# Performance work log

Measured on AMD Instinct MI355X. Metric: run time of the kernel, lower is better.

Reference implementation:

```python
import jax, jax.numpy as jnp
import numpy as np

B, L, DIM = 4, 2048, 1024
EXPAND, D_STATE, D_CONV = 2, 16, 4
D_INNER = EXPAND * DIM          # 2048
DT_RANK = DIM // 16             # 64
MLP_HID = 4 * DIM


def setup_inputs() -> dict:
    key = jax.random.key(0)
    ks = jax.random.split(key, 20)
    s = 0.02
    inp = {
        "hidden_states": jax.random.normal(ks[0], (B, L, DIM), jnp.float32),
        "cond": jax.random.normal(ks[1], (B, DIM), jnp.float32),
        # norm (LayerNorm with affine)
        "norm_w": jnp.ones((DIM,), jnp.float32),
        "norm_b": jnp.zeros((DIM,), jnp.float32),
        # adaLN: Linear(dim, 6*dim)
        "ada_w": jax.random.normal(ks[2], (6 * DIM, DIM), jnp.float32) * s,
        "ada_b": jnp.zeros((6 * DIM,), jnp.float32),
        # Mamba mixer params
        "in_proj_w": jax.random.normal(ks[3], (2 * D_INNER, DIM), jnp.float32) * s,
        "conv_w": jax.random.normal(ks[4], (D_INNER, 1, D_CONV), jnp.float32) * s,
        "conv_b": jnp.zeros((D_INNER,), jnp.float32),
        "x_proj_w": jax.random.normal(ks[5], (DT_RANK + 2 * D_STATE, D_INNER), jnp.float32) * s,
        "dt_proj_w": jax.random.normal(ks[6], (D_INNER, DT_RANK), jnp.float32) * s,
        "dt_proj_b": jax.random.uniform(ks[7], (D_INNER,), jnp.float32, -4.0, -2.0),
        "A_log": jnp.log(jnp.broadcast_to(jnp.arange(1, D_STATE + 1, dtype=jnp.float32), (D_INNER, D_STATE))),
        "Dp": jnp.ones((D_INNER,), jnp.float32),
        "out_proj_w": jax.random.normal(ks[8], (DIM, D_INNER), jnp.float32) * s,
        # MLP
        "fc1_w": jax.random.normal(ks[9], (MLP_HID, DIM), jnp.float32) * s,
        "fc1_b": jnp.zeros((MLP_HID,), jnp.float32),
        "fc2_w": jax.random.normal(ks[10], (DIM, MLP_HID), jnp.float32) * s,
        "fc2_b": jnp.zeros((DIM,), jnp.float32),
    }
    return inp


def _layernorm(x, w, b, eps):
    mu = jnp.mean(x, axis=-1, keepdims=True)
    var = jnp.mean(jnp.square(x - mu), axis=-1, keepdims=True)
    y = (x - mu) * jax.lax.rsqrt(var + eps)
    return y * w + b if w is not None else y


def _modulate(x, shift, scale):
    # x: [B,L,D]; shift/scale: [B,D]
    return x * (1.0 + scale[:, None, :]) + shift[:, None, :]


def _mamba(x_in, in_proj_w, conv_w, conv_b, x_proj_w, dt_proj_w, dt_proj_b, A_log, Dp, out_proj_w):
    # x_in: [B,L,DIM]
    xz = jnp.einsum("bld,ed->ble", x_in, in_proj_w)        # [B,L,2*Di]
    x, z = jnp.split(xz, 2, axis=-1)                        # each [B,L,Di]
    # causal depthwise conv over L
    x_ncl = jnp.transpose(x, (0, 2, 1))                     # [B,Di,L]
    x_ncl = jax.lax.conv_general_dilated(
        x_ncl, conv_w, window_strides=(1,), padding=[(D_CONV - 1, 0)],
        feature_group_count=D_INNER, dimension_numbers=("NCH", "OIH", "NCH"))
    x = jnp.transpose(x_ncl, (0, 2, 1)) + conv_b            # [B,L,Di]
    x = jax.nn.silu(x)
    x_dbl = jnp.einsum("bld,ed->ble", x, x_proj_w)          # [B,L,dt_rank+2*N]
    dt, Bm, Cm = jnp.split(x_dbl, [DT_RANK, DT_RANK + D_STATE], axis=-1)
    dt = jax.nn.softplus(jnp.einsum("blr,dr->bld", dt, dt_proj_w) + dt_proj_b)  # [B,L,Di]
    A = -jnp.exp(A_log)                                     # [Di,N]

    def step(h, inps):
        dt_t, B_t, C_t, x_t = inps                          # [B,Di],[B,N],[B,N],[B,Di]
        dA = jnp.exp(dt_t[..., None] * A)                   # [B,Di,N]
        dBx = (dt_t * x_t)[..., None] * B_t[:, None, :]     # [B,Di,N]
        h = h * dA + dBx
        y = jnp.einsum("bdn,bn->bd", h, C_t)
        return h, y

    h0 = jnp.zeros((x.shape[0], D_INNER, D_STATE), x.dtype)
    xs = (jnp.transpose(dt, (1, 0, 2)), jnp.transpose(Bm, (1, 0, 2)),
          jnp.transpose(Cm, (1, 0, 2)), jnp.transpose(x, (1, 0, 2)))
    _, ys = jax.lax.scan(step, h0, xs)                      # [L,B,Di]
    y = jnp.transpose(ys, (1, 0, 2)) + x * Dp               # [B,L,Di]
    y = y * jax.nn.silu(z)
    return jnp.einsum("bld,od->blo", y, out_proj_w)         # [B,L,DIM]


def reference(hidden_states, cond, norm_w, norm_b, ada_w, ada_b, in_proj_w, conv_w,
              conv_b, x_proj_w, dt_proj_w, dt_proj_b, A_log, Dp, out_proj_w,
              fc1_w, fc1_b, fc2_w, fc2_b):
    residual = hidden_states                                # residual=None path
    hs = _layernorm(residual, norm_w, norm_b, 1e-5)
    mods = jax.nn.silu(cond) @ ada_w.T + ada_b              # [B,6*DIM]
    shift_msa, scale_msa, gate_msa, shift_mlp, scale_mlp, gate_mlp = jnp.split(mods, 6, axis=1)
    hs = gate_msa[:, None, :] * _mamba(_modulate(hs, shift_msa, scale_msa),
                                       in_proj_w, conv_w, conv_b, x_proj_w,
                                       dt_proj_w, dt_proj_b, A_log, Dp, out_proj_w)
    h2 = _modulate(_layernorm(hs, None, None, 1e-6), shift_mlp, scale_mlp)
    h2 = jax.nn.gelu(h2 @ fc1_w.T + fc1_b, approximate=True) @ fc2_w.T + fc2_b
    hs = hs + gate_mlp[:, None, :] * h2
    return (hs, residual)
```

## Files before the change

kernel.cpp:

```cpp
#include <hip/hip_runtime.h>
#include <hip/hip_bf16.h>


typedef unsigned short ushort_t;
typedef __attribute__((ext_vector_type(8))) short short8;
typedef __attribute__((ext_vector_type(4))) float floatx4;
typedef __attribute__((ext_vector_type(4))) unsigned short ushort4v;

#define DEVI __device__ __forceinline__

DEVI float b2f(ushort_t u) { union { unsigned int i; float f; } v; v.i = ((unsigned int)u) << 16; return v.f; }
DEVI ushort_t f2b(float f) {
    union { float f; unsigned int i; } v; v.f = f;
    unsigned int r = v.i + 0x7fffu + ((v.i >> 16) & 1u);
    return (ushort_t)(r >> 16);
}
DEVI float sigmoidf_(float x) { return 1.f / (1.f + __expf(-x)); }
DEVI float siluf_(float x) { return x * sigmoidf_(x); }
DEVI float softplusf_(float x) { return (x > 20.f) ? x : log1pf(__expf(x)); }
DEVI float gelu_tanh_(float x) {
    float c = 0.7978845608028654f * (x + 0.044715f * x * x * x);
    return 0.5f * x * (1.f + tanhf(c));
}
DEVI void async16(ushort_t* lds, const ushort_t* g) {
    __builtin_amdgcn_global_load_lds((const __attribute__((address_space(1))) void*)g,
                                     (__attribute__((address_space(3))) void*)lds,
                                     16, 0, 0);
}

__global__ void detect_kernel(const void* norm_w, int* flag) {
    if (threadIdx.x == 0)
        flag[0] = (((const unsigned int*)norm_w)[0] == 0x3F800000u) ? 1 : 0;
}

__global__ __launch_bounds__(256) void convert_w_kernel(
    const void* __restrict__ src, ushort_t* __restrict__ dst, int n8,
    const int* __restrict__ flag)
{
    int i = blockIdx.x * 256 + threadIdx.x;
    if (i >= n8) return;
    if (*flag) {
        const float4* s = (const float4*)src;
        float4 a = s[2 * i], b = s[2 * i + 1];
        short8 o;
        o[0] = (short)f2b(a.x); o[1] = (short)f2b(a.y);
        o[2] = (short)f2b(a.z); o[3] = (short)f2b(a.w);
        o[4] = (short)f2b(b.x); o[5] = (short)f2b(b.y);
        o[6] = (short)f2b(b.z); o[7] = (short)f2b(b.w);
        ((short8*)dst)[i] = o;
    } else {
        ((short8*)dst)[i] = ((const short8*)src)[i];
    }
}

__global__ __launch_bounds__(256) void canon_bias_kernel(
    const void* __restrict__ src, float* __restrict__ dst, int n,
    const int* __restrict__ flag)
{
    int i = blockIdx.x * 256 + threadIdx.x;
    if (i >= n) return;
    dst[i] = (*flag) ? ((const float*)src)[i] : b2f(((const ushort_t*)src)[i]);
}

__global__ __launch_bounds__(256) void residual_kernel(
    const void* __restrict__ src, void* __restrict__ dst, const int* __restrict__ flag)
{
    size_t i = (size_t)blockIdx.x * 256 + threadIdx.x;
    if (*flag) {
        ((float4*)((float*)dst + 8388608))[i] = ((const float4*)src)[i];
    } else {
        ((ushort4v*)((ushort_t*)dst + 8388608))[i] = ((const ushort4v*)src)[i];
    }
}

__global__ __launch_bounds__(256) void ada_kernel(
    const void* __restrict__ condv, const void* __restrict__ ada_wv,
    const void* __restrict__ ada_bv, float* __restrict__ mods,
    const int* __restrict__ flag)
{
    __shared__ float sc[4096];
    const int tid = threadIdx.x;
    const bool f32 = (*flag != 0);
    if (f32) {
        const float* cf = (const float*)condv;
        for (int i = tid; i < 4096; i += 256) sc[i] = siluf_(cf[i]);
    } else {
        const ushort_t* cb = (const ushort_t*)condv;
        for (int i = tid; i < 4096; i += 256) sc[i] = siluf_(b2f(cb[i]));
    }
    __syncthreads();
    const int j = blockIdx.x * 256 + tid;
    float bb = f32 ? ((const float*)ada_bv)[j] : b2f(((const ushort_t*)ada_bv)[j]);
    float s0 = bb, s1 = bb, s2 = bb, s3 = bb;
    if (f32) {
        const float4* w4 = ((const float4*)ada_wv) + (size_t)j * 256;
        for (int d4 = 0; d4 < 256; d4++) {
            float4 w = w4[d4];
            float wv[4] = {w.x, w.y, w.z, w.w};
#pragma unroll
            for (int e = 0; e < 4; e++) {
                int d = d4 * 4 + e;
                s0 += sc[d] * wv[e];
                s1 += sc[1024 + d] * wv[e];
                s2 += sc[2048 + d] * wv[e];
                s3 += sc[3072 + d] * wv[e];
            }
        }
    } else {
        const ushort_t* wrow = ((const ushort_t*)ada_wv) + (size_t)j * 1024;
        for (int d = 0; d < 1024; d += 8) {
            short8 w8 = *(const short8*)(wrow + d);
#pragma unroll
            for (int e = 0; e < 8; e++) {
                float wv = b2f(((const ushort_t*)&w8)[e]);
                s0 += sc[d + e] * wv;
                s1 += sc[1024 + d + e] * wv;
                s2 += sc[2048 + d + e] * wv;
                s3 += sc[3072 + d + e] * wv;
            }
        }
    }
    mods[0 * 6144 + j] = s0;
    mods[1 * 6144 + j] = s1;
    mods[2 * 6144 + j] = s2;
    mods[3 * 6144 + j] = s3;
}

__global__ __launch_bounds__(256) void ln1_mod_kernel(
    const void* __restrict__ hiddenv, const void* __restrict__ nwv,
    const void* __restrict__ nbv, const float* __restrict__ mods,
    ushort_t* __restrict__ xout, const int* __restrict__ flag)
{
    const int t = blockIdx.x, tid = threadIdx.x;
    const int bb = t >> 11;
    const bool f32 = (*flag != 0);
    float vv[4], s = 0.f, ss = 0.f;
    if (f32) {
        float4 u = ((const float4*)((const float*)hiddenv + (size_t)t * 1024))[tid];
        vv[0] = u.x; vv[1] = u.y; vv[2] = u.z; vv[3] = u.w;
    } else {
        ushort4v u = ((const ushort4v*)((const ushort_t*)hiddenv + (size_t)t * 1024))[tid];
#pragma unroll
        for (int j = 0; j < 4; j++) vv[j] = b2f(u[j]);
    }
#pragma unroll
    for (int j = 0; j < 4; j++) { s += vv[j]; ss += vv[j] * vv[j]; }
#pragma unroll
    for (int off = 32; off > 0; off >>= 1) { s += __shfl_down(s, off); ss += __shfl_down(ss, off); }
    __shared__ float red[8];
    const int wave = tid >> 6, lane = tid & 63;
    if (lane == 0) { red[wave] = s; red[4 + wave] = ss; }
    __syncthreads();
    s = red[0] + red[1] + red[2] + red[3];
    ss = red[4] + red[5] + red[6] + red[7];
    const float mu = s * (1.f / 1024.f);
    const float var = ss * (1.f / 1024.f) - mu * mu;
    const float rstd = rsqrtf(var + 1e-5f);
    const float* mrow = mods + (size_t)bb * 6144;
    ushort4v o;
#pragma unroll
    for (int j = 0; j < 4; j++) {
        int d = tid * 4 + j;
        float w = f32 ? ((const float*)nwv)[d] : b2f(((const ushort_t*)nwv)[d]);
        float b = f32 ? ((const float*)nbv)[d] : b2f(((const ushort_t*)nbv)[d]);
        float y = (vv[j] - mu) * rstd * w + b;
        y = y * (1.f + mrow[1024 + d]) + mrow[d];
        o[j] = f2b(y);
    }
    ((ushort4v*)(xout + (size_t)t * 1024))[tid] = o;
}

__global__ __launch_bounds__(256) void ln2_mod_kernel(
    const ushort_t* __restrict__ hs, const float* __restrict__ mods,
    ushort_t* __restrict__ xout)
{
    const int t = blockIdx.x, tid = threadIdx.x;
    const int bb = t >> 11;
    ushort4v u = ((const ushort4v*)(hs + (size_t)t * 1024))[tid];
    float vv[4], s = 0.f, ss = 0.f;
#pragma unroll
    for (int j = 0; j < 4; j++) { vv[j] = b2f(u[j]); s += vv[j]; ss += vv[j] * vv[j]; }
#pragma unroll
    for (int off = 32; off > 0; off >>= 1) { s += __shfl_down(s, off); ss += __shfl_down(ss, off); }
    __shared__ float red[8];
    const int wave = tid >> 6, lane = tid & 63;
    if (lane == 0) { red[wave] = s; red[4 + wave] = ss; }
    __syncthreads();
    s = red[0] + red[1] + red[2] + red[3];
    ss = red[4] + red[5] + red[6] + red[7];
    const float mu = s * (1.f / 1024.f);
    const float var = ss * (1.f / 1024.f) - mu * mu;
    const float rstd = rsqrtf(var + 1e-6f);
    const float* mrow = mods + (size_t)bb * 6144;
    ushort4v o;
#pragma unroll
    for (int j = 0; j < 4; j++) {
        int d = tid * 4 + j;
        float y = (vv[j] - mu) * rstd;
        y = y * (1.f + mrow[4096 + d]) + mrow[3072 + d];
        o[j] = f2b(y);
    }
    ((ushort4v*)(xout + (size_t)t * 1024))[tid] = o;
}

__global__ __launch_bounds__(256) void conv_silu_kernel(
    const ushort_t* __restrict__ xb, const void* __restrict__ cwv,
    const void* __restrict__ cbv, ushort_t* __restrict__ xc,
    const int* __restrict__ flag)
{
    const int t = blockIdx.x;
    const int l = t & 2047;
    const int c0 = threadIdx.x * 8;
    const bool f32 = (*flag != 0);
    float acc[8];
    float wlf[32];
    if (f32) {
        const float* cbf = (const float*)cbv;
#pragma unroll
        for (int j = 0; j < 8; j++) acc[j] = cbf[c0 + j];
        const float4* cw4 = (const float4*)((const float*)cwv + (size_t)c0 * 4);
#pragma unroll
        for (int q = 0; q < 8; q++) {
            float4 w = cw4[q];
            wlf[q * 4 + 0] = w.x; wlf[q * 4 + 1] = w.y;
            wlf[q * 4 + 2] = w.z; wlf[q * 4 + 3] = w.w;
        }
    } else {
        const ushort_t* cbb = (const ushort_t*)cbv;
#pragma unroll
        for (int j = 0; j < 8; j++) acc[j] = b2f(cbb[c0 + j]);
        const ushort_t* cwb = (const ushort_t*)cwv + (size_t)c0 * 4;
#pragma unroll
        for (int q = 0; q < 32; q++) wlf[q] = b2f(cwb[q]);
    }
#pragma unroll
    for (int k = 0; k < 4; k++) {
        int tl = l + k - 3;
        if (tl < 0) continue;
        short8 xv = *(const short8*)(xb + (size_t)(t + k - 3) * 2048 + c0);
#pragma unroll
        for (int j = 0; j < 8; j++)
            acc[j] += b2f(((const ushort_t*)&xv)[j]) * wlf[j * 4 + k];
    }
    short8 o;
#pragma unroll
    for (int j = 0; j < 8; j++) ((ushort_t*)&o)[j] = f2b(siluf_(acc[j]));
    *(short8*)(xc + (size_t)t * 2048 + c0) = o;
}

__global__ __launch_bounds__(256) void scan_phase1(
    const ushort_t* __restrict__ dtb, const ushort_t* __restrict__ xcv,
    const ushort_t* __restrict__ xdbl, const void* __restrict__ A_logv,
    ushort_t* __restrict__ Hloc, ushort_t* __restrict__ Pst,
    const int* __restrict__ flag)
{
    const int blk = blockIdx.x;
    const int dblk = blk & 7;
    const int c = (blk >> 3) & 31;
    const int b = blk >> 8;
    const int d = dblk * 256 + threadIdx.x;
    const bool f32 = (*flag != 0);
    float Av[16];
#pragma unroll
    for (int n = 0; n < 16; n++) {
        float al = f32 ? ((const float*)A_logv)[(size_t)d * 16 + n]
                       : b2f(((const ushort_t*)A_logv)[(size_t)d * 16 + n]);
        Av[n] = -__expf(al);
    }
    float h[16], Pa[16];
#pragma unroll
    for (int n = 0; n < 16; n++) { h[n] = 0.f; Pa[n] = 1.f; }
    const int t0 = c * 64;
    size_t tb = ((size_t)b * 2048 + t0) * 2048 + d;
    float dtv = b2f(dtb[tb]);
    float xv  = b2f(xcv[tb]);
    for (int tt = 0; tt < 64; ++tt) {
        float dtn = b2f(dtb[tb + 2048]);
        float xn  = b2f(xcv[tb + 2048]);
        const ushort_t* bp = xdbl + ((size_t)b * 2048 + t0 + tt) * 96 + 64;
        short8 B8a = *(const short8*)bp;
        short8 B8b = *(const short8*)(bp + 8);
        float dtx = dtv * xv;
#pragma unroll
        for (int n = 0; n < 8; n++) {
            float dA = __expf(dtv * Av[n]);
            h[n] = h[n] * dA + dtx * b2f(((const ushort_t*)&B8a)[n]);
            Pa[n] *= dA;
        }
#pragma unroll
        for (int n = 8; n < 16; n++) {
            float dA = __expf(dtv * Av[n]);
            h[n] = h[n] * dA + dtx * b2f(((const ushort_t*)&B8b)[n - 8]);
            Pa[n] *= dA;
        }
        dtv = dtn; xv = xn; tb += 2048;
    }
    const size_t o = (((size_t)c * 4 + b) * 16) * 2048 + d;
#pragma unroll
    for (int n = 0; n < 16; n++) {
        Hloc[o + (size_t)n * 2048] = f2b(h[n]);
        Pst [o + (size_t)n * 2048] = f2b(Pa[n]);
    }
}

__global__ __launch_bounds__(256) void scan_phase2(
    const ushort_t* __restrict__ Hloc, const ushort_t* __restrict__ Pst,
    float* __restrict__ Hin)
{
    const int gi = blockIdx.x * 256 + threadIdx.x;
    const int d = gi & 2047;
    const int n = (gi >> 11) & 15;
    const int b = gi >> 15;
    float h = 0.f;
    const size_t o0 = ((size_t)b * 16 + n) * 2048 + d;
    for (int c = 0; c < 32; ++c) {
        const size_t o = o0 + (size_t)c * (4 * 16 * 2048);
        Hin[o] = h;
        h = b2f(Hloc[o]) + b2f(Pst[o]) * h;
    }
}

__global__ __launch_bounds__(256) void scan_phase3(
    const ushort_t* __restrict__ dtb, ushort_t* __restrict__ xc,
    const ushort_t* __restrict__ xdbl, const ushort_t* __restrict__ zbuf,
    const void* __restrict__ A_logv, const void* __restrict__ Dpv,
    const float* __restrict__ Hin, const int* __restrict__ flag)
{
    const int blk = blockIdx.x;
    const int dblk = blk & 7;
    const int c = (blk >> 3) & 31;
    const int b = blk >> 8;
    const int d = dblk * 256 + threadIdx.x;
    const bool f32 = (*flag != 0);
    float Av[16];
#pragma unroll
    for (int n = 0; n < 16; n++) {
        float al = f32 ? ((const float*)A_logv)[(size_t)d * 16 + n]
                       : b2f(((const ushort_t*)A_logv)[(size_t)d * 16 + n]);
        Av[n] = -__expf(al);
    }
    const float Dv = f32 ? ((const float*)Dpv)[d] : b2f(((const ushort_t*)Dpv)[d]);
    float h[16];
    {
        const size_t o = (((size_t)c * 4 + b) * 16) * 2048 + d;
#pragma unroll
        for (int n = 0; n < 16; n++) h[n] = Hin[o + (size_t)n * 2048];
    }
    const int t0 = c * 64;
    size_t tb = ((size_t)b * 2048 + t0) * 2048 + d;
    float dtv = b2f(dtb[tb]);
    float xv  = b2f(xc[tb]);
    float zv  = b2f(zbuf[tb]);
    for (int tt = 0; tt < 64; ++tt) {
        float dtn = b2f(dtb[tb + 2048]);
        float xn  = b2f(xc[tb + 2048]);
        float zn  = b2f(zbuf[tb + 2048]);
        const ushort_t* bp = xdbl + ((size_t)b * 2048 + t0 + tt) * 96 + 64;
        short8 B8a = *(const short8*)bp;
        short8 B8b = *(const short8*)(bp + 8);
        short8 C8a = *(const short8*)(bp + 16);
        short8 C8b = *(const short8*)(bp + 24);
        float dtx = dtv * xv;
        float y = 0.f;
#pragma unroll
        for (int n = 0; n < 8; n++) {
            float dA = __expf(dtv * Av[n]);
            h[n] = h[n] * dA + dtx * b2f(((const ushort_t*)&B8a)[n]);
            y += h[n] * b2f(((const ushort_t*)&C8a)[n]);
        }
#pragma unroll
        for (int n = 8; n < 16; n++) {
            float dA = __expf(dtv * Av[n]);
            h[n] = h[n] * dA + dtx * b2f(((const ushort_t*)&B8b)[n - 8]);
            y += h[n] * b2f(((const ushort_t*)&C8b)[n - 8]);
        }
        float yo = (y + xv * Dv) * siluf_(zv);
        xc[tb] = f2b(yo);
        dtv = dtn; xv = xn; zv = zn; tb += 2048;
    }
}

template <int EPI>
DEVI void epi_store(int row, int col, float v,
                    void* C0, void* C1, int ldc,
                    const float* bias, const float* mods,
                    const ushort_t* hs, int fl)
{
    if constexpr (EPI == 0) {
        if (col < 2048)
            ((ushort_t*)C0)[(size_t)row * 2048 + col] = f2b(v);
        else
            ((ushort_t*)C1)[(size_t)row * 2048 + (col - 2048)] = f2b(v);
    } else if constexpr (EPI == 1) {
        ((ushort_t*)C0)[(size_t)row * ldc + col] = f2b(v);
    } else if constexpr (EPI == 2) {
        v += bias[col];
        ((ushort_t*)C0)[(size_t)row * ldc + col] = f2b(softplusf_(v));
    } else if constexpr (EPI == 3) {
        const int bb = row >> 11;
        v *= mods[(size_t)bb * 6144 + 2048 + col];
        ((ushort_t*)C0)[(size_t)row * ldc + col] = f2b(v);
    } else if constexpr (EPI == 4) {
        v += bias[col];
        ((ushort_t*)C0)[(size_t)row * ldc + col] = f2b(gelu_tanh_(v));
    } else if constexpr (EPI == 5) {
        v += bias[col];
        const int bb = row >> 11;
        float o = b2f(hs[(size_t)row * 1024 + col]) + mods[(size_t)bb * 6144 + 5120 + col] * v;
        if (fl)
            ((float*)C0)[(size_t)row * ldc + col] = o;
        else
            ((ushort_t*)C0)[(size_t)row * ldc + col] = f2b(o);
    }
}

template <int EPI>
__global__ __launch_bounds__(256) void gemm_bt(
    const ushort_t* __restrict__ A, int lda,
    const ushort_t* __restrict__ W,
    int M, int N, int K,
    void* __restrict__ C0, void* __restrict__ C1, int ldc,
    const float* __restrict__ bias,
    const float* __restrict__ mods,
    const ushort_t* __restrict__ hs,
    const int* __restrict__ flag)
{
    __shared__ __align__(16) ushort_t sA[2][128 * 64];
    __shared__ __align__(16) ushort_t sB[2][128 * 64];
    const int tid = threadIdx.x;
    const int wave = tid >> 6, lane = tid & 63;
    const int Mt = M >> 7;
    int bid = blockIdx.x;
    { const int cpx = (int)gridDim.x >> 3; bid = (bid & 7) * cpx + (bid >> 3); }
    const int mt = bid % Mt, nt = bid / Mt;
    const int m0 = mt << 7, n0 = nt << 7;
    const int wr = wave >> 1, wc = wave & 1;
    const int r = tid >> 3, c8 = tid & 7;
    const int rs7 = r & 7;
    int fl = 0;
    if constexpr (EPI == 5) fl = *flag;

    floatx4 acc[4][4];
#pragma unroll
    for (int m = 0; m < 4; m++)
#pragma unroll
        for (int nn = 0; nn < 4; nn++) acc[m][nn] = floatx4{0.f, 0.f, 0.f, 0.f};

    auto stage = [&](int buf, int kt) {
        const int kb = kt << 6;
#pragma unroll
        for (int i = 0; i < 4; i++) {
            const int row = i * 32 + r;
            async16(&sA[buf][(size_t)row * 64 + c8 * 8],
                    A + (size_t)(m0 + row) * lda + kb + ((c8 ^ rs7) << 3));
            int rB = n0 + row; if (rB >= N) rB = N - 1;
            async16(&sB[buf][(size_t)row * 64 + c8 * 8],
                    W + (size_t)rB * K + kb + ((c8 ^ rs7) << 3));
        }
    };
    auto compute = [&](int buf) {
#pragma unroll
        for (int kk = 0; kk < 2; kk++) {
            const int sw = ((kk * 4 + (lane >> 4)) ^ (lane & 7)) << 3;
            short8 bfr[4];
#pragma unroll
            for (int nn = 0; nn < 4; nn++)
                bfr[nn] = *(const short8*)&sB[buf][(size_t)(wc * 64 + nn * 16 + (lane & 15)) * 64 + sw];
#pragma unroll
            for (int m = 0; m < 4; m++) {
                short8 af = *(const short8*)&sA[buf][(size_t)(wr * 64 + m * 16 + (lane & 15)) * 64 + sw];
#pragma unroll
                for (int nn = 0; nn < 4; nn++)
                    acc[m][nn] = __builtin_amdgcn_mfma_f32_16x16x32_bf16(af, bfr[nn], acc[m][nn], 0, 0, 0);
            }
        }
    };

    const int NT = K >> 6;
    stage(0, 0);
    __syncthreads();
    int cur = 0;
    for (int kt = 0; kt < NT - 1; kt++) {
        stage(cur ^ 1, kt + 1);
        compute(cur);
        __syncthreads();
        cur ^= 1;
    }
    compute(cur);

    const int erow = wr * 64 + ((lane >> 4) << 2);
    const int ecol = wc * 64 + (lane & 15);
#pragma unroll
    for (int m = 0; m < 4; m++)
#pragma unroll
        for (int nn = 0; nn < 4; nn++) {
            const int col = n0 + ecol + nn * 16;
            if (col >= N) continue;
#pragma unroll
            for (int rr = 0; rr < 4; rr++)
                epi_store<EPI>(m0 + erow + m * 16 + rr, col, acc[m][nn][rr],
                               C0, C1, ldc, bias, mods, hs, fl);
        }
}

template <int EPI>
__global__ __launch_bounds__(512) void gemm256(
    const ushort_t* __restrict__ A, int lda,
    const ushort_t* __restrict__ W,
    int M, int N, int K,
    void* __restrict__ C0, void* __restrict__ C1, int ldc,
    const float* __restrict__ bias,
    const float* __restrict__ mods,
    const ushort_t* __restrict__ hs,
    const int* __restrict__ flag)
{
    __shared__ __align__(16) ushort_t sA[2][256 * 64];
    __shared__ __align__(16) ushort_t sB[2][256 * 64];
    const int tid = threadIdx.x;
    const int wave = tid >> 6, lane = tid & 63;
    const int Mt = M >> 8;
    int bid = blockIdx.x;
    { const int cpx = (int)gridDim.x >> 3; bid = (bid & 7) * cpx + (bid >> 3); }
    const int mt = bid % Mt, nt = bid / Mt;
    const int m0 = mt << 8, n0 = nt << 8;
    const int wr = wave >> 2, wc = wave & 3;
    const int r = tid >> 3, c8 = tid & 7;
    const int rs7 = r & 7;
    int fl = 0;
    if constexpr (EPI == 5) fl = *flag;

    floatx4 acc[8][4];
#pragma unroll
    for (int m = 0; m < 8; m++)
#pragma unroll
        for (int nn = 0; nn < 4; nn++) acc[m][nn] = floatx4{0.f, 0.f, 0.f, 0.f};

    auto stage = [&](int buf, int kt) {
        const int kb = kt << 6;
#pragma unroll
        for (int i = 0; i < 4; i++) {
            const int row = i * 64 + r;
            async16(&sA[buf][(size_t)row * 64 + c8 * 8],
                    A + (size_t)(m0 + row) * lda + kb + ((c8 ^ rs7) << 3));
            async16(&sB[buf][(size_t)row * 64 + c8 * 8],
                    W + (size_t)(n0 + row) * K + kb + ((c8 ^ rs7) << 3));
        }
    };
    auto compute = [&](int buf) {
#pragma unroll
        for (int kk = 0; kk < 2; kk++) {
            const int sw = ((kk * 4 + (lane >> 4)) ^ (lane & 7)) << 3;
            short8 bfr[4];
#pragma unroll
            for (int nn = 0; nn < 4; nn++)
                bfr[nn] = *(const short8*)&sB[buf][(size_t)(wc * 64 + nn * 16 + (lane & 15)) * 64 + sw];
#pragma unroll
            for (int m = 0; m < 8; m++) {
                short8 af = *(const short8*)&sA[buf][(size_t)(wr * 128 + m * 16 + (lane & 15)) * 64 + sw];
#pragma unroll
                for (int nn = 0; nn < 4; nn++)
                    acc[m][nn] = __builtin_amdgcn_mfma_f32_16x16x32_bf16(af, bfr[nn], acc[m][nn], 0, 0, 0);
            }
        }
    };

    const int NT = K >> 6;
    stage(0, 0);
    __syncthreads();
    int cur = 0;
    for (int kt = 0; kt < NT - 1; kt++) {
        stage(cur ^ 1, kt + 1);
        compute(cur);
        __syncthreads();
        cur ^= 1;
    }
    compute(cur);

    const int erow = wr * 128 + ((lane >> 4) << 2);
    const int ecol = wc * 64 + (lane & 15);
#pragma unroll
    for (int m = 0; m < 8; m++)
#pragma unroll
        for (int nn = 0; nn < 4; nn++) {
            const int col = n0 + ecol + nn * 16;
            if (col >= N) continue;
#pragma unroll
            for (int rr = 0; rr < 4; rr++)
                epi_store<EPI>(m0 + erow + m * 16 + rr, col, acc[m][nn][rr],
                               C0, C1, ldc, bias, mods, hs, fl);
        }
}

extern "C" void kernel_launch(void* const* d_in, const int* in_sizes, int n_in,
                              void* d_out, int out_size, void* d_ws, size_t ws_size,
                              hipStream_t stream)
{
    const void* hidden   = d_in[0];
    const void* cond     = d_in[1];
    const void* norm_w   = d_in[2];
    const void* norm_b   = d_in[3];
    const void* ada_w    = d_in[4];
    const void* ada_b    = d_in[5];
    const void* in_proj  = d_in[6];
    const void* conv_w   = d_in[7];
    const void* conv_b   = d_in[8];
    const void* x_proj   = d_in[9];
    const void* dt_w     = d_in[10];
    const void* dt_b     = d_in[11];
    const void* A_log    = d_in[12];
    const void* Dp       = d_in[13];
    const void* out_proj = d_in[14];
    const void* fc1_w    = d_in[15];
    const void* fc1_b    = d_in[16];
    const void* fc2_w    = d_in[17];
    const void* fc2_b    = d_in[18];

    constexpr size_t OFF_FLAG  = 0;
    constexpr size_t OFF_MODS  = 256;
    constexpr size_t OFF_DTB_F = 131072;
    constexpr size_t OFF_FC1B  = 139264;
    constexpr size_t OFF_FC2B  = 155648;
    constexpr size_t OFF_WIN   = 262144;
    constexpr size_t OFF_WXP   = 8650752;
    constexpr size_t OFF_WDT   = 9043968;
    constexpr size_t OFF_WOUT  = 9306112;
    constexpr size_t OFF_WFC1  = 13500416;
    constexpr size_t OFF_WFC2  = 21889024;
    constexpr size_t OFF_XBUF  = 30277632;
    constexpr size_t OFF_ZBUF  = 63832064;
    constexpr size_t OFF_XCONV = 97386496;
    constexpr size_t OFF_XIN   = 130940928;
    constexpr size_t OFF_XDBL  = 147718144;
    constexpr size_t OFF_HS    = 149291008;
    constexpr size_t WS_NEED   = 166068224;
    if (ws_size < WS_NEED) return;

    char* ws = (char*)d_ws;
    int*      flag   = (int*)(ws + OFF_FLAG);
    float*    mods   = (float*)(ws + OFF_MODS);
    float*    dtb_f  = (float*)(ws + OFF_DTB_F);
    float*    fc1b_f = (float*)(ws + OFF_FC1B);
    float*    fc2b_f = (float*)(ws + OFF_FC2B);
    ushort_t* w_in   = (ushort_t*)(ws + OFF_WIN);
    ushort_t* w_xp   = (ushort_t*)(ws + OFF_WXP);
    ushort_t* w_dt   = (ushort_t*)(ws + OFF_WDT);
    ushort_t* w_out  = (ushort_t*)(ws + OFF_WOUT);
    ushort_t* w_fc1  = (ushort_t*)(ws + OFF_WFC1);
    ushort_t* w_fc2  = (ushort_t*)(ws + OFF_WFC2);
    ushort_t* xbuf   = (ushort_t*)(ws + OFF_XBUF);
    ushort_t* zbuf   = (ushort_t*)(ws + OFF_ZBUF);
    ushort_t* x_conv = (ushort_t*)(ws + OFF_XCONV);
    ushort_t* x_in   = (ushort_t*)(ws + OFF_XIN);
    ushort_t* x_dbl  = (ushort_t*)(ws + OFF_XDBL);
    ushort_t* hsb    = (ushort_t*)(ws + OFF_HS);
    ushort_t* dtb    = xbuf;
    ushort_t* h1     = xbuf;
    ushort_t* h2in   = x_in;
    ushort_t* Hloc   = (ushort_t*)(ws + OFF_XIN);
    ushort_t* Pst    = (ushort_t*)(ws + OFF_XIN + 8388608);
    float*    Hin    = (float*)(ws + OFF_HS);

    detect_kernel<<<1, 64, 0, stream>>>(norm_w, flag);

    convert_w_kernel<<<2048, 256, 0, stream>>>(in_proj, w_in, 524288, flag);
    convert_w_kernel<<<96, 256, 0, stream>>>(x_proj, w_xp, 24576, flag);
    convert_w_kernel<<<64, 256, 0, stream>>>(dt_w, w_dt, 16384, flag);
    convert_w_kernel<<<1024, 256, 0, stream>>>(out_proj, w_out, 262144, flag);
    convert_w_kernel<<<2048, 256, 0, stream>>>(fc1_w, w_fc1, 524288, flag);
    convert_w_kernel<<<2048, 256, 0, stream>>>(fc2_w, w_fc2, 524288, flag);
    canon_bias_kernel<<<8, 256, 0, stream>>>(dt_b, dtb_f, 2048, flag);
    canon_bias_kernel<<<16, 256, 0, stream>>>(fc1_b, fc1b_f, 4096, flag);
    canon_bias_kernel<<<4, 256, 0, stream>>>(fc2_b, fc2b_f, 1024, flag);

    residual_kernel<<<8192, 256, 0, stream>>>(hidden, d_out, flag);

    ada_kernel<<<24, 256, 0, stream>>>(cond, ada_w, ada_b, mods, flag);
    ln1_mod_kernel<<<8192, 256, 0, stream>>>(hidden, norm_w, norm_b, mods, x_in, flag);
    gemm256<0><<<32 * 16, 512, 0, stream>>>(x_in, 1024, w_in, 8192, 4096, 1024,
                                            xbuf, zbuf, 2048, nullptr, nullptr, nullptr, flag);
    conv_silu_kernel<<<8192, 256, 0, stream>>>(xbuf, conv_w, conv_b, x_conv, flag);
    gemm_bt<1><<<64 * 1, 256, 0, stream>>>(x_conv, 2048, w_xp, 8192, 96, 2048,
                                           x_dbl, nullptr, 96, nullptr, nullptr, nullptr, flag);
    gemm_bt<2><<<64 * 16, 256, 0, stream>>>(x_dbl, 96, w_dt, 8192, 2048, 64,
                                            dtb, nullptr, 2048, dtb_f, nullptr, nullptr, flag);
    scan_phase1<<<1024, 256, 0, stream>>>(dtb, x_conv, x_dbl, A_log, Hloc, Pst, flag);
    scan_phase2<<<512, 256, 0, stream>>>(Hloc, Pst, Hin);
    scan_phase3<<<1024, 256, 0, stream>>>(dtb, x_conv, x_dbl, zbuf, A_log, Dp, Hin, flag);
    gemm_bt<3><<<64 * 8, 256, 0, stream>>>(x_conv, 2048, w_out, 8192, 1024, 2048,
                                           hsb, nullptr, 1024, nullptr, mods, nullptr, flag);
    ln2_mod_kernel<<<8192, 256, 0, stream>>>(hsb, mods, h2in);
    gemm256<4><<<32 * 16, 512, 0, stream>>>(h2in, 1024, w_fc1, 8192, 4096, 1024,
                                            h1, nullptr, 4096, fc1b_f, nullptr, nullptr, flag);
    gemm_bt<5><<<64 * 8, 256, 0, stream>>>(h1, 4096, w_fc2, 8192, 1024, 4096,
                                           d_out, nullptr, 1024, fc2b_f, mods, hsb, flag);
}
```

Before: 787.4 us.

## Pipeline GEMM K-loop with explicit vmcnt waits and 8x8 tile swizzle

Replaces the double-buffered GEMM K-loop's __syncthreads with explicit s_waitcnt vmcnt(8) plus raw s_barrier and priority raising around the MFMA compute. Global-to-LDS prefetch of the next tile can then stay in flight while the current tile is consumed. Also remaps workgroup IDs into 8x8 tile groups within each XCD-strided slice to improve L2 reuse of A and W panels. The vmcnt count assumes each thread issues exactly 8 loads per stage, which is fragile if the stage load count differs between the two GEMM variants.

```diff
diff --git a/kernel.cpp b/kernel.cpp
--- a/kernel.cpp
+++ b/kernel.cpp
@@ -26,6 +26,21 @@
     __builtin_amdgcn_global_load_lds((const __attribute__((address_space(1))) void*)g,
                                      (__attribute__((address_space(3))) void*)lds,
                                      16, 0, 0);
+}
+
+DEVI void remap_tile(int bid, int Mt, int Nt, int& mt, int& nt) {
+    const int nwg = Mt * Nt;
+    const int cpx = nwg >> 3;
+    const int v = (bid & 7) * cpx + (bid >> 3);
+    if (((Mt & 7) == 0) && ((Nt & 7) == 0)) {
+        const int s = v >> 6, w = v & 63;
+        const int smt = s % (Mt >> 3), snt = s / (Mt >> 3);
+        mt = smt * 8 + (w >> 3);
+        nt = snt * 8 + (w & 7);
+    } else {
+        mt = v % Mt;
+        nt = v / Mt;
+    }
 }
 
 __global__ void detect_kernel(const void* norm_w, int* flag) {
@@ -414,6 +429,30 @@
     }
 }
 
+#define KLOOP_PIPE(NT)                                               \
+    stage(0, 0);                                                     \
+    {                                                                \
+        int cur = 0;                                                 \
+        for (int kt = 0; kt < (NT); kt++) {                          \
+            if (kt + 1 < (NT)) {                                     \
+                stage(cur ^ 1, kt + 1);                              \
+                asm volatile("s_waitcnt vmcnt(8)" ::: "memory");     \
+            } else {                                                 \
+                asm volatile("s_waitcnt vmcnt(0)" ::: "memory");     \
+            }                                                        \
+            __builtin_amdgcn_sched_barrier(0);                       \
+            __builtin_amdgcn_s_barrier();                            \
+            __builtin_amdgcn_sched_barrier(0);                       \
+            __builtin_amdgcn_s_setprio(1);                           \
+            compute(cur);                                            \
+            __builtin_amdgcn_s_setprio(0);                           \
+            __builtin_amdgcn_sched_barrier(0);                       \
+            __builtin_amdgcn_s_barrier();                            \
+            __builtin_amdgcn_sched_barrier(0);                       \
+            cur ^= 1;                                                \
+        }                                                            \
+    }
+
 template <int EPI>
 __global__ __launch_bounds__(256) void gemm_bt(
     const ushort_t* __restrict__ A, int lda,
@@ -429,10 +468,8 @@
     __shared__ __align__(16) ushort_t sB[2][128 * 64];
     const int tid = threadIdx.x;
     const int wave = tid >> 6, lane = tid & 63;
-    const int Mt = M >> 7;
-    int bid = blockIdx.x;
-    { const int cpx = (int)gridDim.x >> 3; bid = (bid & 7) * cpx + (bid >> 3); }
-    const int mt = bid % Mt, nt = bid / Mt;
+    int mt, nt;
+    remap_tile(blockIdx.x, M >> 7, (N + 127) >> 7, mt, nt);
     const int m0 = mt << 7, n0 = nt << 7;
     const int wr = wave >> 1, wc = wave & 1;
     const int r = tid >> 3, c8 = tid & 7;
@@ -477,16 +514,7 @@
     };
 
     const int NT = K >> 6;
-    stage(0, 0);
-    __syncthreads();
-    int cur = 0;
-    for (int kt = 0; kt < NT - 1; kt++) {
-        stage(cur ^ 1, kt + 1);
-        compute(cur);
-        __syncthreads();
-        cur ^= 1;
-    }
-    compute(cur);
+    KLOOP_PIPE(NT)
 
     const int erow = wr * 64 + ((lane >> 4) << 2);
     const int ecol = wc * 64 + (lane & 15);
@@ -518,10 +546,8 @@
     __shared__ __align__(16) ushort_t sB[2][256 * 64];
     const int tid = threadIdx.x;
     const int wave = tid >> 6, lane = tid & 63;
-    const int Mt = M >> 8;
-    int bid = blockIdx.x;
-    { const int cpx = (int)gridDim.x >> 3; bid = (bid & 7) * cpx + (bid >> 3); }
-    const int mt = bid % Mt, nt = bid / Mt;
+    int mt, nt;
+    remap_tile(blockIdx.x, M >> 8, N >> 8, mt, nt);
     const int m0 = mt << 8, n0 = nt << 8;
     const int wr = wave >> 2, wc = wave & 3;
     const int r = tid >> 3, c8 = tid & 7;
@@ -565,16 +591,7 @@
     };
 
     const int NT = K >> 6;
-    stage(0, 0);
-    __syncthreads();
-    int cur = 0;
-    for (int kt = 0; kt < NT - 1; kt++) {
-        stage(cur ^ 1, kt + 1);
-        compute(cur);
-        __syncthreads();
-        cur ^= 1;
-    }
-    compute(cur);
+    KLOOP_PIPE(NT)
 
     const int erow = wr * 128 + ((lane >> 4) << 2);
     const int ecol = wc * 64 + (lane & 15);
```

New measurement: 775.6 us. Within noise of the previous version (-1.5%).
